# Kernel optimization log

Hardware: AMD Instinct MI355X
Metric: run time of the kernel (lower is better)

Reference implementation:

```python
import jax, jax.numpy as jnp
import numpy as np

N, S, C, K, V = 8, 8192, 1, 1024, 64  # batch, samples, n_channels, n_classes, vec_len


def setup_inputs() -> dict:
    key = jax.random.key(0)
    k1, k2 = jax.random.split(key)
    x0 = jax.random.normal(k1, (N, S, C, V), dtype=jnp.float32)
    embedding0 = jax.random.normal(k2, (C, K, V), dtype=jnp.float32) * 0.001
    return {"x0": x0, "embedding0": embedding0}


def reference(x0, embedding0):
    # normalize=False path of the original module
    x = x0
    emb = embedding0
    Ns = x.shape[0] * x.shape[1]
    xf = x.reshape(Ns, C, V)  # (Ns, C, V)
    # squared distances ||x - e||^2 without materializing (Ns, C, K, V)
    d2 = (
        jnp.sum(xf * xf, axis=-1)[:, :, None]
        - 2.0 * jnp.einsum("ncv,ckv->nck", xf, emb)
        + jnp.sum(emb * emb, axis=-1)[None, :, :]
    )
    index = jnp.argmin(d2, axis=2)  # (Ns, C); argmin of dist == argmin of dist^2
    # histogram entropy (matches torch histc over bins 0..K-1, divided by len(index)=Ns)
    counts = jnp.zeros((K,), jnp.float32).at[index.reshape(-1)].add(1.0)
    prob = counts / Ns
    safe_log = jnp.log(jnp.where(counts > 0, prob, 1.0))
    entropy = -jnp.sum(jnp.where(counts > 0, prob * safe_log, 0.0))
    # gather codewords: embedding[c, index[n,c]]
    output = emb[jnp.arange(C)[None, :], index].reshape(x.shape)
    out0 = jax.lax.stop_gradient(output - x) + x  # straight-through
    out1 = jnp.sum((jax.lax.stop_gradient(x) - output) ** 2, axis=-1)  # (N,S,C)
    out2 = jnp.sum((x - jax.lax.stop_gradient(output)) ** 2, axis=-1)  # (N,S,C)
    return (out0, out1, out2, entropy)
```

## Files before the change

kernel.cpp:

```cpp
#include <hip/hip_runtime.h>
#include <math.h>

#define NS   65536
#define KK   1024
#define VV   64
#define SPB  64
#define NB   (NS / SPB)
#define NW   8
#define TPW  2
#define NPASS 4
#define NMT  (SPB / 16)

#define OUT0_OFF 0
#define OUT1_OFF 4194304
#define OUT2_OFF 4259840
#define ENT_OFF  4325376


typedef __attribute__((ext_vector_type(8))) short bf16x8;
typedef __attribute__((ext_vector_type(4))) float f32x4;

__device__ __forceinline__ short f2bf(float f) {
    unsigned u = __float_as_uint(f);
    u = (u + 0x7fffu + ((u >> 16) & 1u)) >> 16;
    return (short)u;
}

__global__ void vq_prep(const float* __restrict__ emb, unsigned int* __restrict__ hist,
                        float* __restrict__ cinit, short* __restrict__ cb) {
    const int t = blockIdx.x * blockDim.x + threadIdx.x;
    const int c = t >> 3;
    const int g = t & 7;
    if (t < KK) hist[t] = 0u;
    const float* ep = emb + (size_t)c * VV + g * 8;
    float4 f0 = *(const float4*)(ep);
    float4 f1 = *(const float4*)(ep + 4);
    float s = 0.f;
    s=fmaf(f0.x,f0.x,s); s=fmaf(f0.y,f0.y,s); s=fmaf(f0.z,f0.z,s); s=fmaf(f0.w,f0.w,s);
    s=fmaf(f1.x,f1.x,s); s=fmaf(f1.y,f1.y,s); s=fmaf(f1.z,f1.z,s); s=fmaf(f1.w,f1.w,s);
    union { short sh[8]; bf16x8 v; } pk;
    pk.sh[0]=f2bf(f0.x); pk.sh[1]=f2bf(f0.y); pk.sh[2]=f2bf(f0.z); pk.sh[3]=f2bf(f0.w);
    pk.sh[4]=f2bf(f1.x); pk.sh[5]=f2bf(f1.y); pk.sh[6]=f2bf(f1.z); pk.sh[7]=f2bf(f1.w);
    const int T = c >> 4, cc = c & 15;
    short* dst = cb + (size_t)T * 1024 + (g >> 2) * 512 + ((g & 3) * 16 + cc) * 8;
    *(bf16x8*)dst = pk.v;
    s += __shfl_xor(s, 1, 64);
    s += __shfl_xor(s, 2, 64);
    s += __shfl_xor(s, 4, 64);
    if (g == 0) cinit[c] = 1.0f - 0.5f * s;
}

__global__ __launch_bounds__(512, 4) void vq_main(
    const float* __restrict__ x, const float* __restrict__ emb,
    const float* __restrict__ cinit, const short* __restrict__ cb,
    unsigned int* __restrict__ hist,
    float* __restrict__ out0, float* __restrict__ out1, float* __restrict__ out2)
{
    __shared__ __align__(16) char  sA[SPB * 128];
    __shared__ float    sXn[SPB];
    __shared__ unsigned sRed[SPB][NW + 1];
    __shared__ unsigned sPkF[SPB];

    const int tid  = threadIdx.x;
    const int lane = tid & 63;
    const int wv   = tid >> 6;
    const int col  = lane & 15;
    const int quad = lane >> 4;
    const int samp0 = blockIdx.x * SPB;

    {
        const int s = tid >> 3, g = tid & 7;
        const float* xp = x + (size_t)(samp0 + s) * VV + g * 8;
        float4 f0 = *(const float4*)(xp);
        float4 f1 = *(const float4*)(xp + 4);
        float sm = 0.f;
        sm=fmaf(f0.x,f0.x,sm); sm=fmaf(f0.y,f0.y,sm); sm=fmaf(f0.z,f0.z,sm); sm=fmaf(f0.w,f0.w,sm);
        sm=fmaf(f1.x,f1.x,sm); sm=fmaf(f1.y,f1.y,sm); sm=fmaf(f1.z,f1.z,sm); sm=fmaf(f1.w,f1.w,sm);
        union { short sh[8]; bf16x8 v; } pa;
        pa.sh[0]=f2bf(f0.x); pa.sh[1]=f2bf(f0.y); pa.sh[2]=f2bf(f0.z); pa.sh[3]=f2bf(f0.w);
        pa.sh[4]=f2bf(f1.x); pa.sh[5]=f2bf(f1.y); pa.sh[6]=f2bf(f1.z); pa.sh[7]=f2bf(f1.w);
        short* base = (short*)(sA + s * 128);
        *(bf16x8*)(base + ((g ^ (s & 7)) << 3)) = pa.v;
        sm += __shfl_xor(sm, 1, 64);
        sm += __shfl_xor(sm, 2, 64);
        sm += __shfl_xor(sm, 4, 64);
        if ((tid & 7) == 0) sXn[s] = sm;
    }

    const int rb0 = col * 128 + (( quad      ^ (col & 7)) << 4);
    const int rb1 = col * 128 + (((4 + quad) ^ (col & 7)) << 4);

    unsigned pmv[NMT];
    #pragma unroll
    for (int j = 0; j < NMT; ++j) pmv[j] = 0u;

    for (int p = 0; p < NPASS; ++p) {
        bf16x8   af0[TPW], af1[TPW];
        f32x4    cv[TPW];
        unsigned tg[TPW];
        const int Tb = p * 16 + wv * TPW;
        #pragma unroll
        for (int t = 0; t < TPW; ++t) {
            const char* cp = (const char*)cb + (size_t)(Tb + t) * 2048;
            af0[t] = *(const bf16x8*)(cp + lane * 16);
            af1[t] = *(const bf16x8*)(cp + 1024 + lane * 16);
            cv[t]  = *(const f32x4*)(cinit + (Tb + t) * 16 + quad * 4);
            tg[t]  = 1023u - (unsigned)((Tb + t) * 16 + quad * 4);
        }
        if (p == 0) __syncthreads();

        #pragma unroll
        for (int mt = 0; mt < NMT; ++mt) {
            const char* Bp = sA + mt * 2048;
            bf16x8 b0 = *(const bf16x8*)(Bp + rb0);
            bf16x8 b1 = *(const bf16x8*)(Bp + rb1);
            #pragma unroll
            for (int t = 0; t < TPW; ++t) {
                f32x4 acc = __builtin_amdgcn_mfma_f32_16x16x32_bf16(af0[t], b0, cv[t], 0, 0, 0);
                acc       = __builtin_amdgcn_mfma_f32_16x16x32_bf16(af1[t], b1, acc,   0, 0, 0);
                unsigned u0 = ((__float_as_uint(acc[0]) & 0xFFFFFC00u) | tg[t]);
                unsigned u1 = ((__float_as_uint(acc[1]) & 0xFFFFFC00u) | tg[t]) - 1u;
                unsigned u2 = ((__float_as_uint(acc[2]) & 0xFFFFFC00u) | tg[t]) - 2u;
                unsigned u3 = ((__float_as_uint(acc[3]) & 0xFFFFFC00u) | tg[t]) - 3u;
                unsigned m0 = u0 > u1 ? u0 : u1;
                unsigned m1 = u2 > u3 ? u2 : u3;
                unsigned mm = m0 > m1 ? m0 : m1;
                pmv[mt] = pmv[mt] > mm ? pmv[mt] : mm;
            }
        }
    }

    #pragma unroll
    for (int j = 0; j < NMT; ++j) {
        unsigned o;
        o = (unsigned)__shfl_xor((int)pmv[j], 16, 64); pmv[j] = o > pmv[j] ? o : pmv[j];
        o = (unsigned)__shfl_xor((int)pmv[j], 32, 64); pmv[j] = o > pmv[j] ? o : pmv[j];
    }
    {
        unsigned w0 = (quad & 1) ? pmv[1] : pmv[0];
        unsigned w1 = (quad & 1) ? pmv[3] : pmv[2];
        unsigned lo = (quad & 2) ? w1 : w0;
        sRed[quad * 16 + col][wv] = lo;
    }
    __syncthreads();

    if (tid < SPB) {
        unsigned pbest = sRed[tid][0];
        #pragma unroll
        for (int w = 1; w < NW; ++w) {
            unsigned o = sRed[tid][w];
            pbest = o > pbest ? o : pbest;
        }
        sPkF[tid] = pbest;
        int   code = 1023 - (int)(pbest & 1023u);
        float sf   = __uint_as_float(pbest & 0xFFFFFC00u);
        float d    = fmaf(-2.f, sf - 1.0f, sXn[tid]);
        int n = samp0 + tid;
        out1[n] = d;
        out2[n] = d;
        atomicAdd(&hist[code], 1u);
    }
    __syncthreads();

    {
        float4* dstB = (float4*)(out0 + (size_t)samp0 * VV);
        #pragma unroll
        for (int i = 0; i < 2; ++i) {
            const int idx  = i * 512 + tid;
            const int smp  = idx >> 4;
            const int part = idx & 15;
            const int code = 1023 - (int)(sPkF[smp] & 1023u);
            dstB[idx] = *((const float4*)(emb + (size_t)code * VV) + part);
        }
    }
}

__global__ void vq_ent(const unsigned int* __restrict__ hist, float* __restrict__ entOut) {
    __shared__ float sPart[16];
    const int tid  = threadIdx.x;
    const int lane = tid & 63;
    const int wv   = tid >> 6;
    unsigned c = hist[tid];
    float e = 0.f;
    if (c) { float pr = (float)c * (1.0f / (float)NS); e = -pr * logf(pr); }
    #pragma unroll
    for (int off = 32; off > 0; off >>= 1) e += __shfl_down(e, off, 64);
    if (lane == 0) sPart[wv] = e;
    __syncthreads();
    if (tid == 0) {
        float s = 0.f;
        #pragma unroll
        for (int i = 0; i < 16; ++i) s += sPart[i];
        entOut[0] = s;
    }
}

extern "C" void kernel_launch(void* const* d_in, const int* in_sizes, int n_in,
                              void* d_out, int out_size, void* d_ws, size_t ws_size,
                              hipStream_t stream) {
    const float* x   = (const float*)d_in[0];
    const float* emb = (const float*)d_in[1];
    float* out = (float*)d_out;
    unsigned int* hist  = (unsigned int*)d_ws;
    float*        cinit = (float*)((char*)d_ws + 4096);
    short*        cb    = (short*)((char*)d_ws + 8192);

    vq_prep<<<32, 256, 0, stream>>>(emb, hist, cinit, cb);
    vq_main<<<NB, 512, 0, stream>>>(x, emb, cinit, cb, hist,
                                    out + OUT0_OFF, out + OUT1_OFF, out + OUT2_OFF);
    vq_ent<<<1, 1024, 0, stream>>>(hist, out + ENT_OFF);
}
```

Baseline: 94.26 us.

## Preload all codebook fragments per wave once and drop the multi-pass loop

```diff
diff --git a/kernel.cpp b/kernel.cpp
--- a/kernel.cpp
+++ b/kernel.cpp
@@ -7,8 +7,7 @@
 #define SPB  64
 #define NB   (NS / SPB)
 #define NW   8
-#define TPW  2
-#define NPASS 4
+#define TPWF 8
 #define NMT  (SPB / 16)
 
 #define OUT0_OFF 0
@@ -90,43 +89,40 @@
     const int rb0 = col * 128 + (( quad      ^ (col & 7)) << 4);
     const int rb1 = col * 128 + (((4 + quad) ^ (col & 7)) << 4);
 
+    bf16x8 af0[TPWF], af1[TPWF];
+    f32x4  cvv[TPWF];
+    #pragma unroll
+    for (int t = 0; t < TPWF; ++t) {
+        const int T = t * 8 + wv;
+        const char* cp = (const char*)cb + (size_t)T * 2048;
+        af0[t] = *(const bf16x8*)(cp + lane * 16);
+        af1[t] = *(const bf16x8*)(cp + 1024 + lane * 16);
+        cvv[t] = *(const f32x4*)(cinit + T * 16 + quad * 4);
+    }
+    __syncthreads();
+
     unsigned pmv[NMT];
     #pragma unroll
     for (int j = 0; j < NMT; ++j) pmv[j] = 0u;
 
-    for (int p = 0; p < NPASS; ++p) {
-        bf16x8   af0[TPW], af1[TPW];
-        f32x4    cv[TPW];
-        unsigned tg[TPW];
-        const int Tb = p * 16 + wv * TPW;
-        #pragma unroll
-        for (int t = 0; t < TPW; ++t) {
-            const char* cp = (const char*)cb + (size_t)(Tb + t) * 2048;
-            af0[t] = *(const bf16x8*)(cp + lane * 16);
-            af1[t] = *(const bf16x8*)(cp + 1024 + lane * 16);
-            cv[t]  = *(const f32x4*)(cinit + (Tb + t) * 16 + quad * 4);
-            tg[t]  = 1023u - (unsigned)((Tb + t) * 16 + quad * 4);
-        }
-        if (p == 0) __syncthreads();
-
-        #pragma unroll
-        for (int mt = 0; mt < NMT; ++mt) {
-            const char* Bp = sA + mt * 2048;
-            bf16x8 b0 = *(const bf16x8*)(Bp + rb0);
-            bf16x8 b1 = *(const bf16x8*)(Bp + rb1);
-            #pragma unroll
-            for (int t = 0; t < TPW; ++t) {
-                f32x4 acc = __builtin_amdgcn_mfma_f32_16x16x32_bf16(af0[t], b0, cv[t], 0, 0, 0);
-                acc       = __builtin_amdgcn_mfma_f32_16x16x32_bf16(af1[t], b1, acc,   0, 0, 0);
-                unsigned u0 = ((__float_as_uint(acc[0]) & 0xFFFFFC00u) | tg[t]);
-                unsigned u1 = ((__float_as_uint(acc[1]) & 0xFFFFFC00u) | tg[t]) - 1u;
-                unsigned u2 = ((__float_as_uint(acc[2]) & 0xFFFFFC00u) | tg[t]) - 2u;
-                unsigned u3 = ((__float_as_uint(acc[3]) & 0xFFFFFC00u) | tg[t]) - 3u;
-                unsigned m0 = u0 > u1 ? u0 : u1;
-                unsigned m1 = u2 > u3 ? u2 : u3;
-                unsigned mm = m0 > m1 ? m0 : m1;
-                pmv[mt] = pmv[mt] > mm ? pmv[mt] : mm;
-            }
+    #pragma unroll
+    for (int mt = 0; mt < NMT; ++mt) {
+        const char* Bp = sA + mt * 2048;
+        bf16x8 b0 = *(const bf16x8*)(Bp + rb0);
+        bf16x8 b1 = *(const bf16x8*)(Bp + rb1);
+        #pragma unroll
+        for (int t = 0; t < TPWF; ++t) {
+            f32x4 acc = __builtin_amdgcn_mfma_f32_16x16x32_bf16(af0[t], b0, cvv[t], 0, 0, 0);
+            acc       = __builtin_amdgcn_mfma_f32_16x16x32_bf16(af1[t], b1, acc,    0, 0, 0);
+            const unsigned tg = 1023u - (unsigned)((t * 8 + wv) * 16 + quad * 4);
+            unsigned u0 = (__float_as_uint(acc[0]) & 0xFFFFFC00u) | tg;
+            unsigned u1 = (__float_as_uint(acc[1]) & 0xFFFFFC00u) | (tg - 1u);
+            unsigned u2 = (__float_as_uint(acc[2]) & 0xFFFFFC00u) | (tg - 2u);
+            unsigned u3 = (__float_as_uint(acc[3]) & 0xFFFFFC00u) | (tg - 3u);
+            unsigned i0 = u2 > u3 ? u2 : u3;
+            unsigned i1 = i0 > pmv[mt] ? i0 : pmv[mt];
+            unsigned i2 = u0 > u1 ? u0 : u1;
+            pmv[mt] = i2 > i1 ? i2 : i1;
         }
     }
 
```

New measurement: 150.9 us. 60.0% more time.
